# Kernel tuning notes

Hardware: AMD Instinct MI355X
Metric: run time of the kernel (lower is better)

Reference implementation:

```python
import jax, jax.numpy as jnp
import numpy as np

N_CLASSES = 91

def setup_inputs() -> dict:
    key = jax.random.key(0)
    k1, k2 = jax.random.split(key)
    B, H, W = 32, 1024, 1024
    inputs = jax.random.randint(k1, (B, H, W), 0, N_CLASSES, dtype=jnp.int32)
    targets = jax.random.randint(k2, (B, H, W), 0, N_CLASSES, dtype=jnp.int32)
    smooth = jnp.ones((1,), dtype=jnp.float32)  # original default smooth=1
    return {"inputs": inputs, "targets": targets, "smooth": smooth}

def reference(inputs, targets, smooth):
    # Single-pass histogram formulation of the original 91-iteration loop.
    B = inputs.shape[0]
    x = inputs.reshape(B, -1)   # [B, N] int labels
    t = targets.reshape(B, -1)  # [B, N]
    rows = jnp.arange(B)[:, None]
    # per-class counts: cnt_x[b,c] = #pixels with x==c (== a.sum per class)
    cnt_x = jnp.zeros((B, N_CLASSES), jnp.float32).at[rows, x].add(1.0)
    cnt_t = jnp.zeros((B, N_CLASSES), jnp.float32).at[rows, t].add(1.0)
    # intersection[b,c] = #pixels with x==t==c; route mismatches to a dump bin
    match = jnp.where(x == t, x, N_CLASSES)
    inter = jnp.zeros((B, N_CLASSES + 1), jnp.float32).at[rows, match].add(1.0)[:, :N_CLASSES]
    union = cnt_x + cnt_t - inter  # total - intersection
    s = smooth[0]
    iou = (inter + s) / (union + s)  # [B, C]
    return iou.mean(axis=1)          # sum_IoU / n_classes, shape [B]
```

## Files before the change

### kernel.cpp

```cpp
#include <hip/hip_runtime.h>

#define NC 91
#define NB 32
#define HW (1024 * 1024)

#define THREADS 256
#define PPT 64
#define PIX_PER_BLOCK (THREADS * PPT)
#define NCOPY 8


__device__ __forceinline__ void proc_pixel(int x, int t, int* hp, int* s_inter) {
    atomicAdd(&hp[x], x == t ? 2 : 1);
    if (x != t) atomicAdd(&hp[t], 1);
    else        atomicAdd(&s_inter[x], 1);
}

__global__ __launch_bounds__(256, 8) void hist_kernel(const int* __restrict__ x,
                                                      const int* __restrict__ t,
                                                      int* __restrict__ g_hist,
                                                      int* __restrict__ g_inter) {
    __shared__ int s_h[NCOPY * NC];
    __shared__ int s_inter[NC];

    const int tid = threadIdx.x;
    for (int j = tid; j < NCOPY * NC; j += THREADS) s_h[j] = 0;
    if (tid < NC) s_inter[tid] = 0;
    __syncthreads();

    int* hp = &s_h[(tid & 7) * NC];

    const int b = blockIdx.y;
    const long base = (long)b * HW + (long)blockIdx.x * PIX_PER_BLOCK;
    const int4* __restrict__ x4 = (const int4*)(x + base);
    const int4* __restrict__ t4 = (const int4*)(t + base);

    const int n = PPT / 4;
    int4 xv0 = x4[tid],           tv0 = t4[tid];
    int4 xv1 = x4[THREADS + tid], tv1 = t4[THREADS + tid];

    for (int i = 0; i < n; ++i) {
        const int pf = (i + 2 < n) ? (i + 2) : (n - 1);
        int4 xn = x4[pf * THREADS + tid];
        int4 tn = t4[pf * THREADS + tid];

        proc_pixel(xv0.x, tv0.x, hp, s_inter);
        proc_pixel(xv0.y, tv0.y, hp, s_inter);
        proc_pixel(xv0.z, tv0.z, hp, s_inter);
        proc_pixel(xv0.w, tv0.w, hp, s_inter);

        xv0 = xv1; tv0 = tv1;
        xv1 = xn;  tv1 = tn;
    }
    __syncthreads();

    if (tid < NC) {
        int sum = 0;
#pragma unroll
        for (int k = 0; k < NCOPY; ++k) sum += s_h[k * NC + tid];
        if (sum) atomicAdd(&g_hist[b * NC + tid], sum);
        const int in = s_inter[tid];
        if (in)  atomicAdd(&g_inter[b * NC + tid], in);
    }
}

__global__ __launch_bounds__(64) void finalize_kernel(const int* __restrict__ g_hist,
                                                      const int* __restrict__ g_inter,
                                                      const float* __restrict__ smooth,
                                                      float* __restrict__ out) {
    const int b = blockIdx.x;
    const int lane = threadIdx.x;
    const float s = smooth[0];
    float acc = 0.0f;
    for (int c = lane; c < NC; c += 64) {
        float in = (float)g_inter[b * NC + c];
        float ht = (float)g_hist[b * NC + c];
        acc += (in + s) / (ht - in + s);
    }
#pragma unroll
    for (int off = 32; off > 0; off >>= 1)
        acc += __shfl_down(acc, off, 64);
    if (lane == 0) out[b] = acc / (float)NC;
}

extern "C" void kernel_launch(void* const* d_in, const int* in_sizes, int n_in,
                              void* d_out, int out_size, void* d_ws, size_t ws_size,
                              hipStream_t stream) {
    const int* x = (const int*)d_in[0];
    const int* t = (const int*)d_in[1];
    const float* smooth = (const float*)d_in[2];
    float* out = (float*)d_out;

    int* g_hist = (int*)d_ws;
    int* g_inter = g_hist + NB * NC;

    hipMemsetAsync(d_ws, 0, 2 * NB * NC * sizeof(int), stream);

    dim3 grid(HW / PIX_PER_BLOCK, NB);
    hist_kernel<<<grid, THREADS, 0, stream>>>(x, t, g_hist, g_inter);
    finalize_kernel<<<NB, 64, 0, stream>>>(g_hist, g_inter, smooth, out);
}
```

Before: 281.9 us.

## Move target-class histogram to per-block global memory atomics

Target-class counts now go to a per-block, two-copy histogram in global memory, so LDS holds only the input-class histogram and intersection counts. The finalize kernel sums the per-block target partials for each class. The aim is to halve LDS atomic traffic on the shared histogram by moving half the atomics to global/L2. The cost is global atomics to heavily contended addresses, a larger memset, and a serial reduction over 128 entries per class in the finalize kernel.

New measurement: 772.2 us. +173.9%, slower.

```diff
diff --git a/kernel.cpp b/kernel.cpp
--- a/kernel.cpp
+++ b/kernel.cpp
@@ -7,19 +7,16 @@
 #define THREADS 256
 #define PPT 64
 #define PIX_PER_BLOCK (THREADS * PPT)
+#define CHUNKS (HW / PIX_PER_BLOCK)
 #define NCOPY 8
+#define TCOPY 2
 
-
-__device__ __forceinline__ void proc_pixel(int x, int t, int* hp, int* s_inter) {
-    atomicAdd(&hp[x], x == t ? 2 : 1);
-    if (x != t) atomicAdd(&hp[t], 1);
-    else        atomicAdd(&s_inter[x], 1);
-}
 
 __global__ __launch_bounds__(256, 8) void hist_kernel(const int* __restrict__ x,
                                                       const int* __restrict__ t,
                                                       int* __restrict__ g_hist,
-                                                      int* __restrict__ g_inter) {
+                                                      int* __restrict__ g_inter,
+                                                      int* __restrict__ g_t) {
     __shared__ int s_h[NCOPY * NC];
     __shared__ int s_inter[NC];
 
@@ -31,6 +28,9 @@
     int* hp = &s_h[(tid & 7) * NC];
 
     const int b = blockIdx.y;
+    const int blin = b * CHUNKS + blockIdx.x;
+    int* __restrict__ gt = g_t + ((long)blin * TCOPY + (tid >> 7)) * NC;
+
     const long base = (long)b * HW + (long)blockIdx.x * PIX_PER_BLOCK;
     const int4* __restrict__ x4 = (const int4*)(x + base);
     const int4* __restrict__ t4 = (const int4*)(t + base);
@@ -44,10 +44,21 @@
         int4 xn = x4[pf * THREADS + tid];
         int4 tn = t4[pf * THREADS + tid];
 
-        proc_pixel(xv0.x, tv0.x, hp, s_inter);
-        proc_pixel(xv0.y, tv0.y, hp, s_inter);
-        proc_pixel(xv0.z, tv0.z, hp, s_inter);
-        proc_pixel(xv0.w, tv0.w, hp, s_inter);
+        atomicAdd(&hp[xv0.x], 1);
+        atomicAdd(&gt[tv0.x], 1);
+        if (xv0.x == tv0.x) atomicAdd(&s_inter[xv0.x], 1);
+
+        atomicAdd(&hp[xv0.y], 1);
+        atomicAdd(&gt[tv0.y], 1);
+        if (xv0.y == tv0.y) atomicAdd(&s_inter[xv0.y], 1);
+
+        atomicAdd(&hp[xv0.z], 1);
+        atomicAdd(&gt[tv0.z], 1);
+        if (xv0.z == tv0.z) atomicAdd(&s_inter[xv0.z], 1);
+
+        atomicAdd(&hp[xv0.w], 1);
+        atomicAdd(&gt[tv0.w], 1);
+        if (xv0.w == tv0.w) atomicAdd(&s_inter[xv0.w], 1);
 
         xv0 = xv1; tv0 = tv1;
         xv1 = xn;  tv1 = tn;
@@ -66,6 +77,7 @@
 
 __global__ __launch_bounds__(64) void finalize_kernel(const int* __restrict__ g_hist,
                                                       const int* __restrict__ g_inter,
+                                                      const int* __restrict__ g_t,
                                                       const float* __restrict__ smooth,
                                                       float* __restrict__ out) {
     const int b = blockIdx.x;
@@ -73,9 +85,13 @@
     const float s = smooth[0];
     float acc = 0.0f;
     for (int c = lane; c < NC; c += 64) {
-        float in = (float)g_inter[b * NC + c];
-        float ht = (float)g_hist[b * NC + c];
-        acc += (in + s) / (ht - in + s);
+        int cx = g_hist[b * NC + c];
+        int ct = 0;
+        const int* gt = g_t + (long)b * CHUNKS * TCOPY * NC + c;
+        for (int k = 0; k < CHUNKS * TCOPY; ++k)
+            ct += gt[(long)k * NC];
+        int in = g_inter[b * NC + c];
+        acc += ((float)in + s) / ((float)(cx + ct - in) + s);
     }
 #pragma unroll
     for (int off = 32; off > 0; off >>= 1)
@@ -93,10 +109,12 @@
 
     int* g_hist = (int*)d_ws;
     int* g_inter = g_hist + NB * NC;
+    int* g_t = g_inter + NB * NC;
 
-    hipMemsetAsync(d_ws, 0, 2 * NB * NC * sizeof(int), stream);
+    const size_t ws_ints = (size_t)2 * NB * NC + (size_t)NB * CHUNKS * TCOPY * NC;
+    hipMemsetAsync(d_ws, 0, ws_ints * sizeof(int), stream);
 
-    dim3 grid(HW / PIX_PER_BLOCK, NB);
-    hist_kernel<<<grid, THREADS, 0, stream>>>(x, t, g_hist, g_inter);
-    finalize_kernel<<<NB, 64, 0, stream>>>(g_hist, g_inter, smooth, out);
+    dim3 grid(CHUNKS, NB);
+    hist_kernel<<<grid, THREADS, 0, stream>>>(x, t, g_hist, g_inter, g_t);
+    finalize_kernel<<<NB, 64, 0, stream>>>(g_hist, g_inter, g_t, smooth, out);
 }
```

## Replace per-class histograms with a 2D joint (x,t) pair histogram in LDS

Applied to the files above, without the earlier changes.

Each pixel now does a single LDS atomic into a 91x92 joint confusion-matrix histogram instead of two atomics plus an intersection atomic. Row sums, column sums and the diagonal are then reduced into per-class x counts, t counts and intersections, and the finalize step computes the union from them. This targets the cost of issuing several shared-memory atomics per pixel. In exchange it uses about 33KB of LDS per block, lowering occupancy (launch bounds drop from 8 to 4 blocks), zero-fills a much larger table per block, and loses the 8-way replication that spread out contention.

New measurement: 281.6 us. Within noise of the previous version (-0.1%).

```diff
diff --git a/kernel.cpp b/kernel.cpp
--- a/kernel.cpp
+++ b/kernel.cpp
@@ -7,28 +7,20 @@
 #define THREADS 256
 #define PPT 64
 #define PIX_PER_BLOCK (THREADS * PPT)
-#define NCOPY 8
+#define CHUNKS (HW / PIX_PER_BLOCK)
+#define RSTR 92
 
 
-__device__ __forceinline__ void proc_pixel(int x, int t, int* hp, int* s_inter) {
-    atomicAdd(&hp[x], x == t ? 2 : 1);
-    if (x != t) atomicAdd(&hp[t], 1);
-    else        atomicAdd(&s_inter[x], 1);
-}
-
-__global__ __launch_bounds__(256, 8) void hist_kernel(const int* __restrict__ x,
+__global__ __launch_bounds__(256, 4) void hist_kernel(const int* __restrict__ x,
                                                       const int* __restrict__ t,
-                                                      int* __restrict__ g_hist,
-                                                      int* __restrict__ g_inter) {
-    __shared__ int s_h[NCOPY * NC];
-    __shared__ int s_inter[NC];
+                                                      int* __restrict__ g_cx,
+                                                      int* __restrict__ g_ct,
+                                                      int* __restrict__ g_in) {
+    __shared__ __align__(16) int s_pair[NC * RSTR];
 
     const int tid = threadIdx.x;
-    for (int j = tid; j < NCOPY * NC; j += THREADS) s_h[j] = 0;
-    if (tid < NC) s_inter[tid] = 0;
+    for (int j = tid; j < NC * RSTR; j += THREADS) s_pair[j] = 0;
     __syncthreads();
-
-    int* hp = &s_h[(tid & 7) * NC];
 
     const int b = blockIdx.y;
     const long base = (long)b * HW + (long)blockIdx.x * PIX_PER_BLOCK;
@@ -44,10 +36,10 @@
         int4 xn = x4[pf * THREADS + tid];
         int4 tn = t4[pf * THREADS + tid];
 
-        proc_pixel(xv0.x, tv0.x, hp, s_inter);
-        proc_pixel(xv0.y, tv0.y, hp, s_inter);
-        proc_pixel(xv0.z, tv0.z, hp, s_inter);
-        proc_pixel(xv0.w, tv0.w, hp, s_inter);
+        atomicAdd(&s_pair[xv0.x * RSTR + tv0.x], 1);
+        atomicAdd(&s_pair[xv0.y * RSTR + tv0.y], 1);
+        atomicAdd(&s_pair[xv0.z * RSTR + tv0.z], 1);
+        atomicAdd(&s_pair[xv0.w * RSTR + tv0.w], 1);
 
         xv0 = xv1; tv0 = tv1;
         xv1 = xn;  tv1 = tn;
@@ -55,17 +47,28 @@
     __syncthreads();
 
     if (tid < NC) {
-        int sum = 0;
+        int ct = 0;
+        for (int xx = 0; xx < NC; ++xx) ct += s_pair[xx * RSTR + tid];
+        if (ct) atomicAdd(&g_ct[b * NC + tid], ct);
+        const int dg = s_pair[tid * RSTR + tid];
+        if (dg) atomicAdd(&g_in[b * NC + tid], dg);
+    }
+    else if (tid >= 128 && tid < 128 + NC) {
+        const int c = tid - 128;
+        const int4* row = (const int4*)&s_pair[c * RSTR];
+        int cx = 0;
 #pragma unroll
-        for (int k = 0; k < NCOPY; ++k) sum += s_h[k * NC + tid];
-        if (sum) atomicAdd(&g_hist[b * NC + tid], sum);
-        const int in = s_inter[tid];
-        if (in)  atomicAdd(&g_inter[b * NC + tid], in);
+        for (int j = 0; j < RSTR / 4; ++j) {
+            int4 v = row[j];
+            cx += v.x + v.y + v.z + v.w;
+        }
+        if (cx) atomicAdd(&g_cx[b * NC + c], cx);
     }
 }
 
-__global__ __launch_bounds__(64) void finalize_kernel(const int* __restrict__ g_hist,
-                                                      const int* __restrict__ g_inter,
+__global__ __launch_bounds__(64) void finalize_kernel(const int* __restrict__ g_cx,
+                                                      const int* __restrict__ g_ct,
+                                                      const int* __restrict__ g_in,
                                                       const float* __restrict__ smooth,
                                                       float* __restrict__ out) {
     const int b = blockIdx.x;
@@ -73,9 +76,9 @@
     const float s = smooth[0];
     float acc = 0.0f;
     for (int c = lane; c < NC; c += 64) {
-        float in = (float)g_inter[b * NC + c];
-        float ht = (float)g_hist[b * NC + c];
-        acc += (in + s) / (ht - in + s);
+        const float in = (float)g_in[b * NC + c];
+        const float un = (float)(g_cx[b * NC + c] + g_ct[b * NC + c]) - in;
+        acc += (in + s) / (un + s);
     }
 #pragma unroll
     for (int off = 32; off > 0; off >>= 1)
@@ -91,12 +94,13 @@
     const float* smooth = (const float*)d_in[2];
     float* out = (float*)d_out;
 
-    int* g_hist = (int*)d_ws;
-    int* g_inter = g_hist + NB * NC;
+    int* g_cx = (int*)d_ws;
+    int* g_ct = g_cx + NB * NC;
+    int* g_in = g_ct + NB * NC;
 
-    hipMemsetAsync(d_ws, 0, 2 * NB * NC * sizeof(int), stream);
+    hipMemsetAsync(d_ws, 0, 3 * NB * NC * sizeof(int), stream);
 
-    dim3 grid(HW / PIX_PER_BLOCK, NB);
-    hist_kernel<<<grid, THREADS, 0, stream>>>(x, t, g_hist, g_inter);
-    finalize_kernel<<<NB, 64, 0, stream>>>(g_hist, g_inter, smooth, out);
+    dim3 grid(CHUNKS, NB);
+    hist_kernel<<<grid, THREADS, 0, stream>>>(x, t, g_cx, g_ct, g_in);
+    finalize_kernel<<<NB, 64, 0, stream>>>(g_cx, g_ct, g_in, smooth, out);
 }
```
